# Kernel optimization log

Measured on AMD Instinct MI355X. Metric: run time of the kernel, lower is better.

## Reference

```python
import jax, jax.numpy as jnp
import numpy as np

B = 256
DIM = 2048
H = W = 8
SLICE_MAX = 64
SLICE_RANGE = 2
TEMP = 0.1
BN_EPS = 1e-5
COS_EPS = 1e-8


def setup_inputs() -> dict:
    key = jax.random.key(0)
    ks = jax.random.split(key, 6)
    z0 = jax.random.normal(ks[0], (B, DIM, H, W), dtype=jnp.float32)
    z1 = jax.random.normal(ks[1], (B, DIM, H, W), dtype=jnp.float32)
    rel0 = jax.random.randint(ks[2], (B,), 0, SLICE_MAX)
    rel1 = jax.random.randint(ks[3], (B,), 0, SLICE_MAX)
    W1 = jax.random.normal(ks[4], (DIM, DIM), dtype=jnp.float32) * 0.02
    W2 = jax.random.normal(ks[5], (DIM, DIM), dtype=jnp.float32) * 0.02
    return {
        "z0": z0, "z1": z1,
        "rel_slice_idx_0": rel0, "rel_slice_idx_1": rel1,
        "W1": W1, "b1": jnp.zeros((DIM,), jnp.float32),
        "gamma": jnp.ones((DIM,), jnp.float32), "beta": jnp.zeros((DIM,), jnp.float32),
        "W2": W2, "b2": jnp.zeros((DIM,), jnp.float32),
    }


def _projection_head(z, W1, b1, gamma, beta, W2, b2):
    # AdaptiveAvgPool2d(1) + Flatten: [N, C, H, W] -> [N, C]
    p = jnp.mean(z, axis=(2, 3))
    h = p @ W1.T + b1
    # BatchNorm1d in training mode: batch statistics (biased variance)
    mu = jnp.mean(h, axis=0)
    var = jnp.var(h, axis=0)
    h = (h - mu) * jax.lax.rsqrt(var + BN_EPS) * gamma + beta
    h = jax.nn.relu(h)
    return h @ W2.T + b2


def reference(z0, z1, rel_slice_idx_0, rel_slice_idx_1, W1, b1, gamma, beta, W2, b2):
    # domain_contrast=True -> rel_slice_idx = rel_slice_idx_0 only
    rel = rel_slice_idx_0
    z = jnp.concatenate([z0, z1], axis=0)           # [2B, C, H, W]
    z = _projection_head(z, W1, b1, gamma, beta, W2, b2)  # [2B, DIM]

    # full cosine-similarity matrix (fused, instead of the per-row python loop)
    norms = jnp.maximum(jnp.linalg.norm(z, axis=1, keepdims=True), COS_EPS)
    zn = z / norms
    sim = zn @ zn.T                                  # [2B, 2B]
    # similarity_weighting='none' -> weights == 1
    S = jnp.exp(sim / TEMP)

    # relative-position pos/neg masks over the first B (same-domain) samples
    diff = jnp.abs(rel[:, None] - rel[None, :])      # [B, B]
    eye = jnp.eye(B, dtype=bool)
    pos_mask = (diff <= SLICE_RANGE) & (~eye)
    neg_mask = diff > SLICE_RANGE

    S_bb = S[:B, :B]
    # negatives = same-domain negatives + ALL other-domain samples (domain_contrast)
    neg_sum = jnp.sum(S_bb * neg_mask, axis=1) + jnp.sum(S[:B, B:], axis=1)  # [B]

    terms = -jnp.log(S_bb / (S_bb + neg_sum[:, None]))  # [B, B]
    cnt = jnp.sum(pos_mask, axis=1)
    loss_b = jnp.sum(terms * pos_mask, axis=1) / jnp.maximum(cnt, 1)
    defined = cnt > 0
    loss = jnp.sum(jnp.where(defined, loss_b, 0.0))
    n_defined = jnp.sum(defined)
    return loss, n_defined
```

## Files before the change

### kernel.cpp

```cpp
#include <hip/hip_runtime.h>

typedef __attribute__((ext_vector_type(8))) short s8v;
typedef __attribute__((ext_vector_type(4))) short s4v;
typedef __attribute__((ext_vector_type(4))) float f4v;

#define DIM 2048
#define NROW 512
#define NB 256

__device__ inline short f2bf(float f) {
    union { float f; unsigned int u; } v; v.f = f;
    unsigned int u = v.u;
    unsigned int r = (u + 0x7fffu + ((u >> 16) & 1u)) >> 16;
    return (short)r;
}

__device__ __forceinline__ int pk_trunc(float a, float b) {
    return __builtin_amdgcn_perm(__float_as_uint(b), __float_as_uint(a), 0x07060302);
}

__global__ __launch_bounds__(256) void pool_kernel(const float* __restrict__ z0,
                                                   const float* __restrict__ z1,
                                                   short* __restrict__ p) {
    int t = threadIdx.x;
    int c = blockIdx.x;
    float4 v[8], w[8];
    const float* src = (c < 4096) ? z0 + (long)c * 8192 : z1 + (long)(c - 4096) * 8192;
#pragma unroll
    for (int i = 0; i < 8; ++i) v[i] = *(const float4*)(src + i * 1024 + t * 4);
#pragma unroll
    for (int it = 0; it < 4; ++it) {
        int cn = c + 2048;
        if (it < 3) {
            const float* s2 = (cn < 4096) ? z0 + (long)cn * 8192 : z1 + (long)(cn - 4096) * 8192;
#pragma unroll
            for (int i = 0; i < 8; ++i) w[i] = *(const float4*)(s2 + i * 1024 + t * 4);
        }
        int pairBase = c * 128;
#pragma unroll
        for (int i = 0; i < 8; ++i) {
            float s = v[i].x + v[i].y + v[i].z + v[i].w;
            s += __shfl_xor(s, 1);
            s += __shfl_xor(s, 2);
            s += __shfl_xor(s, 4);
            s += __shfl_xor(s, 8);
            if ((t & 15) == 0) p[pairBase + i * 16 + (t >> 4)] = f2bf(s * (1.0f / 64.0f));
        }
        c = cn;
#pragma unroll
        for (int i = 0; i < 8; ++i) v[i] = w[i];
    }
}

__device__ __forceinline__ int swz(int r, int k) { return r * 256 + (k ^ ((r & 7) << 3)); }

__global__ __launch_bounds__(256) void gemm_ks(const short* __restrict__ A,
                                               const short* __restrict__ Bh,
                                               const float* __restrict__ Bf,
                                               const float* __restrict__ bias,
                                               float* __restrict__ C,
                                               float* __restrict__ stats,
                                               int M, int N, int K, int kChunk) {
    __shared__ short sm[2 * 64 * 256];
    short* lA = sm;
    short* lB = sm + 64 * 256;
    int t = threadIdx.x;
    int n0 = blockIdx.x * 64, m0 = blockIdx.y * 64;
    int kbase = blockIdx.z * kChunk;
    long zoff = (long)blockIdx.z * M * N;
    int lane = t & 63, w = t >> 6;
    int l16 = lane & 15, quad = lane >> 4;
    int ks = w * 64;
    f4v acc[4][4] = {};
    int sr = t >> 3;
    int sq8 = (t & 7) * 8;

    for (int it = 0; it < kChunk; it += 256) {
        int k0 = kbase + it;
#pragma unroll
        for (int pp = 0; pp < 2; ++pp) {
            int r = sr + pp * 32;
            const short* as = &A[(long)(m0 + r) * K + k0];
#pragma unroll
            for (int j = 0; j < 4; ++j)
                *(s8v*)&lA[swz(r, sq8 + j * 64)] = *(const s8v*)&as[sq8 + j * 64];
        }
        if (Bh) {
#pragma unroll
            for (int pp = 0; pp < 2; ++pp) {
                int r = sr + pp * 32;
                const short* bs = &Bh[(long)(n0 + r) * K + k0];
#pragma unroll
                for (int j = 0; j < 4; ++j)
                    *(s8v*)&lB[swz(r, sq8 + j * 64)] = *(const s8v*)&bs[sq8 + j * 64];
            }
        } else {
#pragma unroll
            for (int pp = 0; pp < 2; ++pp) {
                int r = sr + pp * 32;
                const float* bs = &Bf[(long)(n0 + r) * K + k0];
#pragma unroll
                for (int j = 0; j < 4; ++j) {
                    float4 x = *(const float4*)&bs[sq8 + j * 64];
                    float4 y = *(const float4*)&bs[sq8 + j * 64 + 4];
                    int4 o;
                    o.x = pk_trunc(x.x, x.y);
                    o.y = pk_trunc(x.z, x.w);
                    o.z = pk_trunc(y.x, y.y);
                    o.w = pk_trunc(y.z, y.w);
                    *(int4*)&lB[swz(r, sq8 + j * 64)] = o;
                }
            }
        }
        __syncthreads();
#pragma unroll
        for (int kk = 0; kk < 2; ++kk) {
            s8v af[4], bf[4];
#pragma unroll
            for (int i = 0; i < 4; ++i)
                af[i] = *(const s8v*)&lA[swz(i * 16 + l16, ks + kk * 32 + quad * 8)];
#pragma unroll
            for (int j = 0; j < 4; ++j)
                bf[j] = *(const s8v*)&lB[swz(j * 16 + l16, ks + kk * 32 + quad * 8)];
#pragma unroll
            for (int i = 0; i < 4; ++i)
#pragma unroll
                for (int j = 0; j < 4; ++j)
                    acc[i][j] = __builtin_amdgcn_mfma_f32_16x16x32_bf16(af[i], bf[j], acc[i][j], 0, 0, 0);
        }
        __syncthreads();
    }

    float* fr = (float*)sm;
#pragma unroll
    for (int i = 0; i < 4; ++i)
#pragma unroll
        for (int j = 0; j < 4; ++j)
#pragma unroll
            for (int r = 0; r < 4; ++r)
                fr[w * 4096 + (i * 16 + quad * 4 + r) * 64 + j * 16 + l16] = acc[i][j][r];
    __syncthreads();
    int c = t & 63;
    int rbase = (t >> 6) * 16;
    float bv = bias ? bias[n0 + c] : 0.0f;
    float s = 0.f, q = 0.f;
#pragma unroll
    for (int r = 0; r < 16; ++r) {
        int rr = rbase + r;
        float h = fr[rr * 64 + c] + fr[4096 + rr * 64 + c]
                + fr[8192 + rr * 64 + c] + fr[12288 + rr * 64 + c] + bv;
        C[zoff + (long)(m0 + rr) * N + n0 + c] = h;
        s += h; q += h * h;
    }
    if (stats) {
        __syncthreads();
        fr[(t >> 6) * 64 + c] = s;
        fr[256 + (t >> 6) * 64 + c] = q;
        __syncthreads();
        if (t < 64) {
            float ss = fr[t] + fr[64 + t] + fr[128 + t] + fr[192 + t];
            float qq = fr[256 + t] + fr[320 + t] + fr[384 + t] + fr[448 + t];
            atomicAdd(&stats[n0 + t], ss);
            atomicAdd(&stats[2048 + n0 + t], qq);
        }
    }
}

__global__ __launch_bounds__(256) void bn_finalize(const float* __restrict__ stats,
                                                   const float* __restrict__ gamma,
                                                   const float* __restrict__ beta,
                                                   float* __restrict__ scale,
                                                   float* __restrict__ shift) {
    int c = blockIdx.x * 256 + threadIdx.x;
    float mu = stats[c] * (1.0f / NROW);
    float var = stats[2048 + c] * (1.0f / NROW) - mu * mu;
    float sc = gamma[c] * rsqrtf(var + 1e-5f);
    scale[c] = sc;
    shift[c] = beta[c] - mu * sc;
}

__global__ __launch_bounds__(256) void bn_relu_cast(const float* __restrict__ h,
                                                    const float* __restrict__ scale,
                                                    const float* __restrict__ shift,
                                                    short* __restrict__ hn) {
    int idx = (blockIdx.x * 256 + threadIdx.x) * 4;
    int col = idx & (DIM - 1);
    float4 v = *(const float4*)(h + idx);
    float4 sc = *(const float4*)(scale + col);
    float4 sh = *(const float4*)(shift + col);
    s4v o;
    o.x = f2bf(fmaxf(v.x * sc.x + sh.x, 0.f));
    o.y = f2bf(fmaxf(v.y * sc.y + sh.y, 0.f));
    o.z = f2bf(fmaxf(v.z * sc.z + sh.z, 0.f));
    o.w = f2bf(fmaxf(v.w * sc.w + sh.w, 0.f));
    *(s4v*)(hn + idx) = o;
}

__global__ __launch_bounds__(256) void rownorm(const float* __restrict__ z,
                                               short* __restrict__ zn) {
    __shared__ float red[4];
    int row = blockIdx.x, t = threadIdx.x;
    const float* zr = z + (long)row * DIM;
    float4 v0 = *(const float4*)(zr + t * 4);
    float4 v1 = *(const float4*)(zr + 1024 + t * 4);
    float ss = v0.x * v0.x + v0.y * v0.y + v0.z * v0.z + v0.w * v0.w
             + v1.x * v1.x + v1.y * v1.y + v1.z * v1.z + v1.w * v1.w;
#pragma unroll
    for (int m = 1; m < 64; m <<= 1) ss += __shfl_xor(ss, m);
    if ((t & 63) == 0) red[t >> 6] = ss;
    __syncthreads();
    float tot = red[0] + red[1] + red[2] + red[3];
    float inv = 1.0f / fmaxf(sqrtf(tot), 1e-8f);
    s4v a, b;
    a.x = f2bf(v0.x * inv); a.y = f2bf(v0.y * inv); a.z = f2bf(v0.z * inv); a.w = f2bf(v0.w * inv);
    b.x = f2bf(v1.x * inv); b.y = f2bf(v1.y * inv); b.z = f2bf(v1.z * inv); b.w = f2bf(v1.w * inv);
    *(s4v*)(zn + (long)row * DIM + t * 4) = a;
    *(s4v*)(zn + (long)row * DIM + 1024 + t * 4) = b;
}

__global__ __launch_bounds__(256) void ksum8(const float* __restrict__ simp,
                                             float* __restrict__ sim,
                                             float* __restrict__ out) {
    int idx = (blockIdx.x * 256 + threadIdx.x) * 4;
    float4 o = {0.f, 0.f, 0.f, 0.f};
#pragma unroll
    for (int z = 0; z < 8; ++z) {
        float4 a = *(const float4*)(simp + (long)z * 131072 + idx);
        o.x += a.x; o.y += a.y; o.z += a.z; o.w += a.w;
    }
    *(float4*)(sim + idx) = o;
    if (blockIdx.x == 0 && threadIdx.x == 0) { out[0] = 0.f; out[1] = 0.f; }
}

__global__ __launch_bounds__(256) void loss_kernel(const float* __restrict__ sim,
                                                   const int* __restrict__ rel,
                                                   float* __restrict__ out) {
    __shared__ float lsum[4];
    __shared__ float lcnt[4];
    int t = threadIdx.x, lane = t & 63, wave = t >> 6;
    int i = blockIdx.x * 4 + wave;
    int reli = rel[i];
    float s[8];
    float neg = 0.f;
#pragma unroll
    for (int kk = 0; kk < 8; ++kk) {
        int j = lane + kk * 64;
        s[kk] = sim[i * 512 + j];
        float e = __expf(10.0f * s[kk]);
        if (j >= NB || abs(reli - rel[j]) > 2) neg += e;
    }
#pragma unroll
    for (int m = 1; m < 64; m <<= 1) neg += __shfl_xor(neg, m);
    float ts = 0.f; int cnt = 0;
#pragma unroll
    for (int kk = 0; kk < 4; ++kk) {
        int j = lane + kk * 64;
        if (j != i && abs(reli - rel[j]) <= 2) {
            ts += logf(__expf(10.0f * s[kk]) + neg) - 10.0f * s[kk];
            cnt++;
        }
    }
#pragma unroll
    for (int m = 1; m < 64; m <<= 1) {
        ts += __shfl_xor(ts, m);
        cnt += __shfl_xor(cnt, m);
    }
    if (lane == 0) {
        lsum[wave] = (cnt > 0) ? ts / (float)cnt : 0.f;
        lcnt[wave] = (cnt > 0) ? 1.f : 0.f;
    }
    __syncthreads();
    if (t == 0) {
        atomicAdd(&out[0], lsum[0] + lsum[1] + lsum[2] + lsum[3]);
        atomicAdd(&out[1], lcnt[0] + lcnt[1] + lcnt[2] + lcnt[3]);
    }
}

extern "C" void kernel_launch(void* const* d_in, const int* in_sizes, int n_in,
                              void* d_out, int out_size, void* d_ws, size_t ws_size,
                              hipStream_t stream) {
    const float* z0    = (const float*)d_in[0];
    const float* z1    = (const float*)d_in[1];
    const int*   rel0  = (const int*)d_in[2];
    const float* W1    = (const float*)d_in[4];
    const float* b1    = (const float*)d_in[5];
    const float* gamma = (const float*)d_in[6];
    const float* beta  = (const float*)d_in[7];
    const float* W2    = (const float*)d_in[8];
    const float* b2    = (const float*)d_in[9];

    char* ws = (char*)d_ws;
    short* p_bf  = (short*)(ws);
    float* h     = (float*)(ws + (2l  << 20));
    short* hn    = (short*)(ws + (6l  << 20));
    float* zproj = (float*)(ws + (8l  << 20));
    short* zn    = (short*)(ws + (12l << 20));
    float* simp  = (float*)(ws + (14l << 20));
    float* sim   = (float*)(ws + (18l << 20));
    float* stats = (float*)(ws + (19l << 20));
    float* scale = (float*)(ws + (19l << 20) + 16384);
    float* shift = (float*)(ws + (19l << 20) + 24576);

    hipMemsetAsync(stats, 0, 16384, stream);
    pool_kernel<<<2048, 256, 0, stream>>>(z0, z1, p_bf);
    gemm_ks<<<dim3(32, 8, 1), 256, 0, stream>>>(p_bf, nullptr, W1, b1, h, stats,
                                                NROW, DIM, DIM, DIM);
    bn_finalize<<<8, 256, 0, stream>>>(stats, gamma, beta, scale, shift);
    bn_relu_cast<<<1024, 256, 0, stream>>>(h, scale, shift, hn);
    gemm_ks<<<dim3(32, 8, 1), 256, 0, stream>>>(hn, nullptr, W2, b2, zproj, nullptr,
                                                NROW, DIM, DIM, DIM);
    rownorm<<<512, 256, 0, stream>>>(zproj, zn);
    gemm_ks<<<dim3(8, 4, 8), 256, 0, stream>>>(zn, zn, nullptr, nullptr, simp, nullptr,
                                               NB, NROW, DIM, 256);
    ksum8<<<128, 256, 0, stream>>>(simp, sim, (float*)d_out);
    loss_kernel<<<64, 256, 0, stream>>>(sim, rel0, (float*)d_out);
}
```

Before: 372.9 us.

## Restructure pooling kernel: one chunk per block, DPP quad reduction, packed bf16 stores

The pooling kernel now runs 8192 blocks that each handle one 8192-float chunk, replacing 2048 blocks that looped over four chunks with manual register double-buffering. Each group of four threads owns two adjacent channels, so the reduction is a 4-lane DPP quad sum instead of a 16-lane shuffle tree. The two bf16 results are written as one packed 32-bit store. The aim is to raise memory-level parallelism and cut shuffle and store overhead in this bandwidth-bound stage, at the cost of a less coalesced per-thread access pattern (strided 16-byte loads within each 512-byte channel).

Result: no change. 366.6 us (-1.7%).

```diff
diff --git a/kernel.cpp b/kernel.cpp
--- a/kernel.cpp
+++ b/kernel.cpp
@@ -19,36 +19,36 @@
     return __builtin_amdgcn_perm(__float_as_uint(b), __float_as_uint(a), 0x07060302);
 }
 
+__device__ __forceinline__ float qsum(float s) {
+    int i = __float_as_int(s);
+    s += __int_as_float(__builtin_amdgcn_update_dpp(i, i, 0xB1, 0xF, 0xF, false));
+    i = __float_as_int(s);
+    s += __int_as_float(__builtin_amdgcn_update_dpp(i, i, 0x4E, 0xF, 0xF, false));
+    return s;
+}
+
 __global__ __launch_bounds__(256) void pool_kernel(const float* __restrict__ z0,
                                                    const float* __restrict__ z1,
                                                    short* __restrict__ p) {
     int t = threadIdx.x;
     int c = blockIdx.x;
-    float4 v[8], w[8];
     const float* src = (c < 4096) ? z0 + (long)c * 8192 : z1 + (long)(c - 4096) * 8192;
-#pragma unroll
-    for (int i = 0; i < 8; ++i) v[i] = *(const float4*)(src + i * 1024 + t * 4);
-#pragma unroll
-    for (int it = 0; it < 4; ++it) {
-        int cn = c + 2048;
-        if (it < 3) {
-            const float* s2 = (cn < 4096) ? z0 + (long)cn * 8192 : z1 + (long)(cn - 4096) * 8192;
-#pragma unroll
-            for (int i = 0; i < 8; ++i) w[i] = *(const float4*)(s2 + i * 1024 + t * 4);
-        }
-        int pairBase = c * 128;
-#pragma unroll
-        for (int i = 0; i < 8; ++i) {
-            float s = v[i].x + v[i].y + v[i].z + v[i].w;
-            s += __shfl_xor(s, 1);
-            s += __shfl_xor(s, 2);
-            s += __shfl_xor(s, 4);
-            s += __shfl_xor(s, 8);
-            if ((t & 15) == 0) p[pairBase + i * 16 + (t >> 4)] = f2bf(s * (1.0f / 64.0f));
-        }
-        c = cn;
-#pragma unroll
-        for (int i = 0; i < 8; ++i) v[i] = w[i];
+    int g = t >> 2, sub = t & 3;
+    const float* base = src + g * 128 + sub * 4;
+    float4 v[8];
+#pragma unroll
+    for (int j = 0; j < 8; ++j) v[j] = *(const float4*)(base + j * 16);
+    float sA = 0.f, sB = 0.f;
+#pragma unroll
+    for (int j = 0; j < 4; ++j) sA += v[j].x + v[j].y + v[j].z + v[j].w;
+#pragma unroll
+    for (int j = 4; j < 8; ++j) sB += v[j].x + v[j].y + v[j].z + v[j].w;
+    sA = qsum(sA);
+    sB = qsum(sB);
+    if (sub == 0) {
+        int pk = (int)(unsigned short)f2bf(sA * (1.0f / 64.0f))
+               | ((int)(unsigned short)f2bf(sB * (1.0f / 64.0f)) << 16);
+        ((int*)p)[c * 64 + g] = pk;
     }
 }
 
@@ -302,7 +302,7 @@
     float* shift = (float*)(ws + (19l << 20) + 24576);
 
     hipMemsetAsync(stats, 0, 16384, stream);
-    pool_kernel<<<2048, 256, 0, stream>>>(z0, z1, p_bf);
+    pool_kernel<<<8192, 256, 0, stream>>>(z0, z1, p_bf);
     gemm_ks<<<dim3(32, 8, 1), 256, 0, stream>>>(p_bf, nullptr, W1, b1, h, stats,
                                                 NROW, DIM, DIM, DIM);
     bn_finalize<<<8, 256, 0, stream>>>(stats, gamma, beta, scale, shift);
```
